# Kernel tuning notes

Hardware: AMD Instinct MI355X
Metric: run time of the kernel (lower is better)

The kernel has to match this reference:

```python
import jax, jax.numpy as jnp
import numpy as np

# dims
B, NB, T, NC = 16, 55, 512, 8          # batch, filter bands, time steps, CSP comps
D, L, H, E, K, F, C = 512, 6, 8, 8, 2, 2048, 2  # embed, depth, heads, experts, top_k, d_ff, classes
DH = D // H
IN = NB * NC  # 440
EPS = 1e-5


def _ln(x, s, b):
    m = x.mean(-1, keepdims=True)
    v = ((x - m) ** 2).mean(-1, keepdims=True)
    return (x - m) / jnp.sqrt(v + EPS) * s + b


def setup_inputs() -> dict:
    key = jax.random.key(0)
    ks = iter(jax.random.split(key, 64))
    n = lambda shape, s=0.02: jax.random.normal(next(ks), shape, jnp.float32) * s
    inp = {
        "x": jax.random.normal(next(ks), (B, NB, T, NC), jnp.float32),
        # frontend
        "proj_w": n((IN, D)), "proj_b": jnp.zeros((D,), jnp.float32),
        "pos": n((1, T, D)),
        "ln_pre_s": jnp.ones((D,), jnp.float32), "ln_pre_b": jnp.zeros((D,), jnp.float32),
        # stacked transformer-block params [L, ...]
        "ln1_s": jnp.ones((L, D), jnp.float32), "ln1_b": jnp.zeros((L, D), jnp.float32),
        "wq": n((L, D, D)), "bq": jnp.zeros((L, D), jnp.float32),
        "wk": n((L, D, D)), "bk": jnp.zeros((L, D), jnp.float32),
        "wv": n((L, D, D)), "bv": jnp.zeros((L, D), jnp.float32),
        "wo": n((L, D, D)), "bo": jnp.zeros((L, D), jnp.float32),
        "ln2_s": jnp.ones((L, D), jnp.float32), "ln2_b": jnp.zeros((L, D), jnp.float32),
        "gate_w": n((L, D, E)),
        "e_w1": n((L, E, D, F)), "e_b1": jnp.zeros((L, E, F), jnp.float32),
        "e_w2": n((L, E, F, D)), "e_b2": jnp.zeros((L, E, D), jnp.float32),
        # classifier head
        "ln_f_s": jnp.ones((D,), jnp.float32), "ln_f_b": jnp.zeros((D,), jnp.float32),
        "head_w": n((D, C)), "head_b": jnp.zeros((C,), jnp.float32),
    }
    return inp


def _moe(h, gw, w1, b1, w2, b2):
    # h: [N, D]; top-K softmax-gated mixture of GELU-FFN experts + load-balance aux loss
    N = h.shape[0]
    probs = jax.nn.softmax(h @ gw, axis=-1)                  # [N, E]
    vals, idx = jax.lax.top_k(probs, K)                      # [N, K]
    w = vals / vals.sum(-1, keepdims=True)                   # renormalized top-k weights
    disp = jax.nn.one_hot(idx, E, dtype=h.dtype)             # [N, K, E]
    combine = (disp * w[..., None]).sum(1)                   # [N, E]
    y = jnp.zeros_like(h)
    for e in range(E):  # small fixed expert loop
        y = y + combine[:, e:e + 1] * (jax.nn.gelu(h @ w1[e] + b1[e]) @ w2[e] + b2[e])
    frac = disp.mean((0, 1)) * K                             # fraction of tokens routed to each expert
    aux = E * jnp.sum(frac * probs.mean(0))
    return y, aux


def reference(x, proj_w, proj_b, pos, ln_pre_s, ln_pre_b, ln1_s, ln1_b, wq, bq, wk, bk,
              wv, bv, wo, bo, ln2_s, ln2_b, gate_w, e_w1, e_b1, e_w2, e_b2,
              ln_f_s, ln_f_b, head_w, head_b):
    b, nb, t, nc = x.shape
    h = x.transpose(0, 2, 1, 3).reshape(b, t, nb * nc) @ proj_w + proj_b  # [B,T,D]
    h = _ln(h + pos[:, :t, :], ln_pre_s, ln_pre_b)
    scale = DH ** -0.5
    total_aux = jnp.float32(0.0)
    for l in range(L):
        # pre-LN multi-head self-attention
        a = _ln(h, ln1_s[l], ln1_b[l])
        q = (a @ wq[l] + bq[l]).reshape(b, t, H, DH)
        k = (a @ wk[l] + bk[l]).reshape(b, t, H, DH)
        v = (a @ wv[l] + bv[l]).reshape(b, t, H, DH)
        att = jax.nn.softmax(jnp.einsum('bqhd,bkhd->bhqk', q, k) * scale, axis=-1)
        o = jnp.einsum('bhqk,bkhd->bqhd', att, v).reshape(b, t, D) @ wo[l] + bo[l]
        h = h + o
        # pre-LN MoE FFN
        m = _ln(h, ln2_s[l], ln2_b[l]).reshape(b * t, D)
        y, aux = _moe(m, gate_w[l], e_w1[l], e_b1[l], e_w2[l], e_b2[l])
        h = h + y.reshape(b, t, D)
        total_aux = total_aux + aux
    pooled = h.mean(axis=1)                                   # [B, D]
    logits = _ln(pooled, ln_f_s, ln_f_b) @ head_w + head_b    # [B, C]
    return logits, total_aux
```

## Files before the change

### kernel.cpp

```cpp
#include <hip/hip_runtime.h>
#include <stdint.h>

typedef unsigned short u16;
typedef unsigned int   u32;
typedef short bh8 __attribute__((ext_vector_type(8)));
typedef float f4  __attribute__((ext_vector_type(4)));

#define NTOK    8192
#define PADROWS 17408
#define MAXTILES 136

__device__ __forceinline__ u16 f2bf(float f){
  u32 u = __float_as_uint(f);
  return (u16)((u + 0x7fffu + ((u>>16)&1u)) >> 16);
}
__device__ __forceinline__ float bf2f(u16 h){ return __uint_as_float(((u32)h)<<16); }
__device__ __forceinline__ u32 pk2(float a, float b){ return (u32)f2bf(a) | ((u32)f2bf(b)<<16); }
__device__ __forceinline__ float gelu_f(float x){
  float u = 0.7978845608028654f*(x + 0.044715f*x*x*x);
  float t = 1.f - 2.f/(__expf(2.f*u)+1.f);
  return 0.5f*x*(1.f+t);
}
__device__ __forceinline__ void gload_lds16(const void* g, void* l){
  __builtin_amdgcn_global_load_lds((const __attribute__((address_space(1))) u32*)g,
                                   (__attribute__((address_space(3))) u32*)l, 16, 0, 0);
}

__global__ __launch_bounds__(256) void xpose_k(const float* __restrict__ x, u16* __restrict__ xt){
  int idx = blockIdx.x*256 + threadIdx.x;
  const float* src = x + (size_t)idx*8;
  float4 a = *(const float4*)src;
  float4 b = *(const float4*)(src+4);
  int t  = idx & 511;
  int nb = (idx>>9) % 55;
  int bb = (idx>>9) / 55;
  uint4 u;
  u.x = pk2(a.x,a.y); u.y = pk2(a.z,a.w); u.z = pk2(b.x,b.y); u.w = pk2(b.z,b.w);
  *(uint4*)&xt[((size_t)(bb*512+t))*448 + nb*8] = u;
}

__device__ __forceinline__ void tile_xpose(const float* __restrict__ src, u16* __restrict__ dst,
                                           int Ksrc, int N, int Kdst, float (*tile)[65])
{
  int tid = threadIdx.x;
  int k0 = blockIdx.y*64, n0 = blockIdx.x*64;
  #pragma unroll
  for (int p=0;p<4;++p){
    int r = p*16 + (tid>>4);
    int c4 = (tid&15)*4;
    int k = k0 + r;
    float4 v = (k < Ksrc) ? *(const float4*)&src[(size_t)k*N + n0 + c4] : (float4){0.f,0.f,0.f,0.f};
    tile[r][c4]=v.x; tile[r][c4+1]=v.y; tile[r][c4+2]=v.z; tile[r][c4+3]=v.w;
  }
  __syncthreads();
  #pragma unroll
  for (int p=0;p<2;++p){
    int rn = p*32 + (tid>>3);
    int ck = (tid&7)*8;
    uint4 u;
    u.x = pk2(tile[ck+0][rn], tile[ck+1][rn]);
    u.y = pk2(tile[ck+2][rn], tile[ck+3][rn]);
    u.z = pk2(tile[ck+4][rn], tile[ck+5][rn]);
    u.w = pk2(tile[ck+6][rn], tile[ck+7][rn]);
    *(uint4*)&dst[(size_t)(n0+rn)*Kdst + k0 + ck] = u;
  }
}

__global__ __launch_bounds__(256) void wconv_k(const float* __restrict__ src, u16* __restrict__ dst,
                                               int Ksrc, int N, int Kdst){
  __shared__ float tile[64][65];
  src += (size_t)blockIdx.z*Ksrc*N;
  dst += (size_t)blockIdx.z*N*Kdst;
  tile_xpose(src, dst, Ksrc, N, Kdst, tile);
}

__global__ __launch_bounds__(256) void wconv4_k(const float* __restrict__ wq, const float* __restrict__ wk,
    const float* __restrict__ wv, const float* __restrict__ wo,
    u16* __restrict__ qkvt, u16* __restrict__ wot)
{
  __shared__ float tile[64][65];
  int z = blockIdx.z;
  const float* src = (z==0)? wq : (z==1)? wk : (z==2)? wv : wo;
  u16* dst = (z==3) ? wot : qkvt + (size_t)z*512*512;
  tile_xpose(src, dst, 512, 512, 512, tile);
}

__global__ __launch_bounds__(256) void qkvb_k(const float* __restrict__ bq, const float* __restrict__ bk,
                                              const float* __restrict__ bv, float* __restrict__ qkvb){
  int idx = blockIdx.x*256 + threadIdx.x;
  int l = idx/1536, c = idx - l*1536;
  const float* s = (c<512)? bq : (c<1024)? bk : bv;
  qkvb[idx] = s[l*512 + (c&511)];
}

template<int MODE, bool GATHER>
__global__ __launch_bounds__(256) void gemm2_k(
    const u16* __restrict__ A, int lda,
    const u16* __restrict__ Bt, int ldb, int Ksteps,
    const float* __restrict__ biasBase,
    float* __restrict__ Cf, u16* __restrict__ Cb, int ldc,
    const int* __restrict__ tile_e, const int* __restrict__ toklist,
    const float* __restrict__ wlist, int expN)
{
  __shared__ __align__(16) u16 As[2][128*32];
  __shared__ __align__(16) u16 Bs[2][128*32];
  const int tid = threadIdx.x, lane = tid&63, w = tid>>6;
  const int wr = w>>1, wc = w&1;
  int nx = gridDim.x;
  int nwg = nx * gridDim.y;
  int lin = blockIdx.y*nx + blockIdx.x;
  int qq = nwg>>3, rr = nwg&7, xc = lin&7, oo = lin>>3;
  int wg = (xc<rr ? xc*(qq+1) : rr*(qq+1)+(xc-rr)*qq) + oo;
  int by = wg/nx, bx = wg - by*nx;
  const int n0 = bx*128, m0 = by*128;
  const u16* Bp = Bt;
  const float* bias = biasBase;
  if constexpr (MODE>=3){
    int e = tile_e[by];
    Bp   += (size_t)e*(size_t)expN*(size_t)ldb;
    bias += (size_t)e*(size_t)expN;
  }
  const u16* asrc0; const u16* asrc1; const u16* bsrc0; const u16* bsrc1;
  {
    int idx0 = tid, row0 = idx0>>2, sp0 = idx0&3, ks0 = sp0 ^ ((row0>>1)&3);
    int idx1 = 256+tid, row1 = idx1>>2, sp1 = idx1&3, ks1 = sp1 ^ ((row1>>1)&3);
    size_t ar0 = GATHER ? (size_t)toklist[m0+row0] : (size_t)(m0+row0);
    size_t ar1 = GATHER ? (size_t)toklist[m0+row1] : (size_t)(m0+row1);
    asrc0 = A + ar0*(size_t)lda + ks0*8;
    asrc1 = A + ar1*(size_t)lda + ks1*8;
    bsrc0 = Bp + (size_t)(n0+row0)*ldb + ks0*8;
    bsrc1 = Bp + (size_t)(n0+row1)*ldb + ks1*8;
  }
  f4 acc[4][4];
  #pragma unroll
  for (int i=0;i<4;++i)
    #pragma unroll
    for (int j=0;j<4;++j) acc[i][j] = (f4){0.f,0.f,0.f,0.f};

  gload_lds16(asrc0, &As[0][tid*8]);
  gload_lds16(asrc1, &As[0][(256+tid)*8]);
  gload_lds16(bsrc0, &Bs[0][tid*8]);
  gload_lds16(bsrc1, &Bs[0][(256+tid)*8]);
  asrc0 += 32; asrc1 += 32; bsrc0 += 32; bsrc1 += 32;
  __syncthreads();

  int buf = 0;
  for (int kt=0; kt<Ksteps; ++kt){
    if (kt+1 < Ksteps){
      int nb = buf^1;
      gload_lds16(asrc0, &As[nb][tid*8]);
      gload_lds16(asrc1, &As[nb][(256+tid)*8]);
      gload_lds16(bsrc0, &Bs[nb][tid*8]);
      gload_lds16(bsrc1, &Bs[nb][(256+tid)*8]);
      asrc0 += 32; asrc1 += 32; bsrc0 += 32; bsrc1 += 32;
    }
    bh8 af[4], bf[4];
    const int q = lane>>4;
    #pragma unroll
    for (int mf=0;mf<4;++mf){
      int r = wr*64 + mf*16 + (lane&15);
      af[mf] = *(const bh8*)&As[buf][r*32 + (q ^ ((r>>1)&3))*8];
    }
    #pragma unroll
    for (int nf=0;nf<4;++nf){
      int r = wc*64 + nf*16 + (lane&15);
      bf[nf] = *(const bh8*)&Bs[buf][r*32 + (q ^ ((r>>1)&3))*8];
    }
    #pragma unroll
    for (int mf=0;mf<4;++mf)
      #pragma unroll
      for (int nf=0;nf<4;++nf)
        acc[mf][nf] = __builtin_amdgcn_mfma_f32_16x16x32_bf16(af[mf], bf[nf], acc[mf][nf], 0, 0, 0);
    __syncthreads();
    buf ^= 1;
  }
  #pragma unroll
  for (int mf=0;mf<4;++mf){
    #pragma unroll
    for (int nf=0;nf<4;++nf){
      f4 d = acc[mf][nf];
      int ncol = n0 + wc*64 + nf*16 + (lane&15);
      float bv = bias[ncol];
      #pragma unroll
      for (int r=0;r<4;++r){
        int mrow = m0 + wr*64 + mf*16 + (lane>>4)*4 + r;
        float val = d[r] + bv;
        if constexpr (MODE==0){
          Cf[(size_t)mrow*ldc + ncol] = val;
        } else if constexpr (MODE==1){
          int slab = ncol>>6, dh = ncol&63;
          Cb[((size_t)slab*NTOK + (size_t)mrow)*64 + dh] = f2bf(val);
        } else if constexpr (MODE==2){
          Cf[(size_t)mrow*ldc + ncol] += val;
        } else if constexpr (MODE==3){
          Cb[(size_t)mrow*ldc + ncol] = f2bf(gelu_f(val));
        } else {
          Cb[(size_t)mrow*ldc + ncol] = f2bf(wlist[mrow]*val);
        }
      }
    }
  }
}

template<bool ADDPOS, bool OUTF32>
__global__ __launch_bounds__(256) void ln_k(const float* __restrict__ X, const float* __restrict__ pos,
    const float* __restrict__ sc, const float* __restrict__ bi,
    float* __restrict__ outF, u16* __restrict__ outB)
{
  int tid=threadIdx.x, lane=tid&63, w=tid>>6;
  int row = blockIdx.x*4 + w;
  const float* xr = X + (size_t)row*512 + lane*8;
  float x[8];
  float4 v0 = *(const float4*)xr;
  float4 v1 = *(const float4*)(xr+4);
  x[0]=v0.x;x[1]=v0.y;x[2]=v0.z;x[3]=v0.w;x[4]=v1.x;x[5]=v1.y;x[6]=v1.z;x[7]=v1.w;
  if constexpr (ADDPOS){
    const float* pr = pos + (size_t)(row&511)*512 + lane*8;
    float4 p0 = *(const float4*)pr, p1 = *(const float4*)(pr+4);
    x[0]+=p0.x;x[1]+=p0.y;x[2]+=p0.z;x[3]+=p0.w;x[4]+=p1.x;x[5]+=p1.y;x[6]+=p1.z;x[7]+=p1.w;
  }
  float sm=0.f, sq=0.f;
  #pragma unroll
  for (int i=0;i<8;++i){ sm+=x[i]; sq+=x[i]*x[i]; }
  #pragma unroll
  for (int mk=1; mk<64; mk<<=1){ sm += __shfl_xor(sm, mk); sq += __shfl_xor(sq, mk); }
  float mean = sm*(1.f/512.f);
  float var  = sq*(1.f/512.f) - mean*mean;
  float rstd = rsqrtf(var + 1e-5f);
  int d0 = lane*8;
  float4 s0 = *(const float4*)(sc+d0), s1 = *(const float4*)(sc+d0+4);
  float4 b0 = *(const float4*)(bi+d0), b1 = *(const float4*)(bi+d0+4);
  float y[8];
  y[0]=(x[0]-mean)*rstd*s0.x+b0.x; y[1]=(x[1]-mean)*rstd*s0.y+b0.y;
  y[2]=(x[2]-mean)*rstd*s0.z+b0.z; y[3]=(x[3]-mean)*rstd*s0.w+b0.w;
  y[4]=(x[4]-mean)*rstd*s1.x+b1.x; y[5]=(x[5]-mean)*rstd*s1.y+b1.y;
  y[6]=(x[6]-mean)*rstd*s1.z+b1.z; y[7]=(x[7]-mean)*rstd*s1.w+b1.w;
  if constexpr (OUTF32){
    float4 o0 = {y[0],y[1],y[2],y[3]}, o1 = {y[4],y[5],y[6],y[7]};
    *(float4*)(outF + (size_t)row*512 + d0)     = o0;
    *(float4*)(outF + (size_t)row*512 + d0 + 4) = o1;
  } else {
    uint4 u; u.x=pk2(y[0],y[1]); u.y=pk2(y[2],y[3]); u.z=pk2(y[4],y[5]); u.w=pk2(y[6],y[7]);
    *(uint4*)&outB[(size_t)row*512 + d0] = u;
  }
}

__global__ __launch_bounds__(256) void attn_k(const u16* __restrict__ QKV, u16* __restrict__ Og)
{
  __shared__ __align__(16) u16 VT[2][64*72];
  __shared__ __align__(16) u16 PS[4][16*72];
  int tid=threadIdx.x, lane=tid&63, w=tid>>6;
  int qt=blockIdx.x, hh=blockIdx.y, bb=blockIdx.z;
  const u16* Qh = QKV + ((size_t)hh     *NTOK + (size_t)bb*512)*64;
  const u16* Kh = QKV + ((size_t)(8+hh) *NTOK + (size_t)bb*512)*64;
  const u16* Vh = QKV + ((size_t)(16+hh)*NTOK + (size_t)bb*512)*64;
  size_t obase = (size_t)bb*512*512 + (size_t)hh*64;
  int qrow0 = qt*64 + w*16;
  bh8 qf[2];
  #pragma unroll
  for (int kf=0;kf<2;++kf)
    qf[kf] = *(const bh8*)&Qh[ (size_t)(qrow0 + (lane&15))*64 + kf*32 + (lane>>4)*8 ];
  f4 oacc[4];
  #pragma unroll
  for (int i=0;i<4;++i) oacc[i] = (f4){0.f,0.f,0.f,0.f};
  float mrun[4] = {-1e30f,-1e30f,-1e30f,-1e30f};
  float lrun[4] = {0.f,0.f,0.f,0.f};
  const float scale = 0.125f;

  for (int kt=0; kt<8; ++kt){
    const int buf = kt&1;
    #pragma unroll
    for (int r2=0;r2<2;++r2){
      int idx = r2*256 + tid;
      int dhg = idx&7;
      int dh0 = dhg*8, key = idx>>3;
      uint4 raw = *(const uint4*)&Vh[ (size_t)(kt*64+key)*64 + dh0 ];
      int kx = key ^ (dhg<<3);
      u32 rw[4] = {raw.x, raw.y, raw.z, raw.w};
      #pragma unroll
      for (int j=0;j<4;++j){
        VT[buf][(dh0+2*j  )*72 + kx] = (u16)(rw[j]&0xffff);
        VT[buf][(dh0+2*j+1)*72 + kx] = (u16)(rw[j]>>16);
      }
    }
    f4 s[4];
    #pragma unroll
    for (int nf=0;nf<4;++nf){
      size_t krow = (size_t)(kt*64+nf*16+(lane&15))*64 + (lane>>4)*8;
      bh8 k0 = *(const bh8*)&Kh[krow];
      bh8 k1 = *(const bh8*)&Kh[krow+32];
      f4 z = (f4){0.f,0.f,0.f,0.f};
      z = __builtin_amdgcn_mfma_f32_16x16x32_bf16(qf[0], k0, z, 0,0,0);
      z = __builtin_amdgcn_mfma_f32_16x16x32_bf16(qf[1], k1, z, 0,0,0);
      s[nf] = z;
    }
    float pe[4][4];
    #pragma unroll
    for (int r=0;r<4;++r){
      float sv0=s[0][r]*scale, sv1=s[1][r]*scale, sv2=s[2][r]*scale, sv3=s[3][r]*scale;
      float mt = fmaxf(fmaxf(sv0,sv1), fmaxf(sv2,sv3));
      #pragma unroll
      for (int mk=1; mk<16; mk<<=1) mt = fmaxf(mt, __shfl_xor(mt, mk));
      float mn = fmaxf(mrun[r], mt);
      float sf = __expf(mrun[r]-mn);
      float p0=__expf(sv0-mn), p1=__expf(sv1-mn), p2=__expf(sv2-mn), p3=__expf(sv3-mn);
      pe[0][r]=p0; pe[1][r]=p1; pe[2][r]=p2; pe[3][r]=p3;
      float rs = p0+p1+p2+p3;
      #pragma unroll
      for (int mk=1; mk<16; mk<<=1) rs += __shfl_xor(rs, mk);
      lrun[r] = lrun[r]*sf + rs;
      mrun[r] = mn;
      #pragma unroll
      for (int df=0;df<4;++df) oacc[df][r] *= sf;
    }
    #pragma unroll
    for (int nf=0;nf<4;++nf)
      #pragma unroll
      for (int r=0;r<4;++r)
        PS[w][ ((lane>>4)*4+r)*72 + nf*16 + (lane&15) ] = f2bf(pe[nf][r]);
    __syncthreads();
    #pragma unroll
    for (int ks=0;ks<2;++ks){
      bh8 pa = *(const bh8*)&PS[w][ (lane&15)*72 + ks*32 + (lane>>4)*8 ];
      #pragma unroll
      for (int df=0;df<4;++df){
        int dh = df*16 + (lane&15);
        int sgrp = (dh>>3)&7;
        bh8 vb = *(const bh8*)&VT[buf][ dh*72 + ((ks*4 + (lane>>4)) ^ sgrp)*8 ];
        oacc[df] = __builtin_amdgcn_mfma_f32_16x16x32_bf16(pa, vb, oacc[df], 0,0,0);
      }
    }
  }
  #pragma unroll
  for (int df=0;df<4;++df)
    #pragma unroll
    for (int r=0;r<4;++r){
      int qr = qrow0 + (lane>>4)*4 + r;
      float ov = oacc[df][r] / lrun[r];
      Og[ obase + (size_t)qr*512 + df*16 + (lane&15) ] = f2bf(ov);
    }
}

__global__ __launch_bounds__(256) void route_k(const u16* __restrict__ m, const float* __restrict__ gw,
    float* __restrict__ psum, int* __restrict__ cnt, int* __restrict__ t2e, float* __restrict__ t2w)
{
  __shared__ float ps[8]; __shared__ int cs[8];
  int tid=threadIdx.x, lane=tid&63, w=tid>>6;
  if (tid<8){ ps[tid]=0.f; cs[tid]=0; }
  __syncthreads();
  for (int it=0; it<4; ++it){
    int t = blockIdx.x*16 + w*4 + it;
    const u16* row = m + (size_t)t*512 + lane*8;
    uint4 raw = *(const uint4*)row;
    u32 rw[4] = {raw.x,raw.y,raw.z,raw.w};
    float x[8];
    #pragma unroll
    for (int j=0;j<4;++j){ x[2*j]=bf2f((u16)(rw[j]&0xffff)); x[2*j+1]=bf2f((u16)(rw[j]>>16)); }
    float acc[8] = {0,0,0,0,0,0,0,0};
    #pragma unroll
    for (int j=0;j<8;++j){
      const float* g = gw + (size_t)(lane*8+j)*8;
      float4 g0 = *(const float4*)g, g1 = *(const float4*)(g+4);
      acc[0]+=x[j]*g0.x; acc[1]+=x[j]*g0.y; acc[2]+=x[j]*g0.z; acc[3]+=x[j]*g0.w;
      acc[4]+=x[j]*g1.x; acc[5]+=x[j]*g1.y; acc[6]+=x[j]*g1.z; acc[7]+=x[j]*g1.w;
    }
    #pragma unroll
    for (int mk=1; mk<64; mk<<=1)
      #pragma unroll
      for (int e=0;e<8;++e) acc[e] += __shfl_xor(acc[e], mk);
    if (lane==0){
      float mx=acc[0];
      #pragma unroll
      for (int e=1;e<8;++e) mx = fmaxf(mx, acc[e]);
      float pe[8], tot=0.f;
      #pragma unroll
      for (int e=0;e<8;++e){ pe[e]=__expf(acc[e]-mx); tot+=pe[e]; }
      float inv = 1.f/tot;
      #pragma unroll
      for (int e=0;e<8;++e) pe[e]*=inv;
      int e0=0; float v0=pe[0];
      #pragma unroll
      for (int e=1;e<8;++e) if (pe[e]>v0){ v0=pe[e]; e0=e; }
      int e1=-1; float v1=-1.f;
      #pragma unroll
      for (int e=0;e<8;++e) if (e!=e0 && pe[e]>v1){ v1=pe[e]; e1=e; }
      float invw = 1.f/(v0+v1);
      t2e[2*t]=e0; t2w[2*t]=v0*invw; t2e[2*t+1]=e1; t2w[2*t+1]=v1*invw;
      #pragma unroll
      for (int e=0;e<8;++e) atomicAdd(&ps[e], pe[e]);
      atomicAdd(&cs[e0],1); atomicAdd(&cs[e1],1);
    }
  }
  __syncthreads();
  if (tid<8){ atomicAdd(&psum[tid], ps[tid]); atomicAdd(&cnt[tid], cs[tid]); }
}

__global__ __launch_bounds__(256) void offsets_k(const int* __restrict__ cnt, const float* __restrict__ psum,
    int* __restrict__ offs, int* __restrict__ fill, int* __restrict__ tile_e,
    int* __restrict__ toklist, float* __restrict__ wlist, float* __restrict__ auxp)
{
  int tid = threadIdx.x;
  if (tid==0){
    int off=0; float auxl=0.f;
    for (int e=0;e<8;++e){
      offs[e] = off;
      int reg = (cnt[e]+127)&~127;
      int t0 = off>>7, t1 = (off+reg)>>7;
      for (int t=t0;t<t1;++t) tile_e[t]=e;
      off += reg;
      auxl += ((float)cnt[e]*(1.f/8192.f)) * (psum[e]*(1.f/8192.f));
    }
    for (int t=off>>7; t<MAXTILES; ++t) tile_e[t]=0;
    auxp[0] += 8.f*auxl;
  }
  if (tid<8) fill[tid]=0;
  for (int i=tid;i<PADROWS;i+=256){ toklist[i]=0; wlist[i]=0.f; }
}

__global__ __launch_bounds__(256) void scatter_k(const int* __restrict__ t2e, const float* __restrict__ t2w,
    const int* __restrict__ offs, int* __restrict__ fill,
    int* __restrict__ toklist, float* __restrict__ wlist, int* __restrict__ t2pos)
{
  int t = blockIdx.x*256 + threadIdx.x;
  #pragma unroll
  for (int kk=0;kk<2;++kk){
    int e = t2e[2*t+kk];
    int p = atomicAdd(&fill[e], 1);
    int i = offs[e] + p;
    toklist[i] = t; wlist[i] = t2w[2*t+kk]; t2pos[2*t+kk] = i;
  }
}

__global__ __launch_bounds__(256) void gather_k(float* __restrict__ h, const u16* __restrict__ yb,
                                                const int* __restrict__ t2pos)
{
  int tid = threadIdx.x;
  int t = blockIdx.x*4 + (tid>>6);
  int lane = tid&63;
  int p0 = t2pos[2*t], p1 = t2pos[2*t+1];
  uint4 a = *(const uint4*)&yb[(size_t)p0*512 + lane*8];
  uint4 b = *(const uint4*)&yb[(size_t)p1*512 + lane*8];
  float* hp = h + (size_t)t*512 + lane*8;
  float4 h0 = *(float4*)hp, h1 = *(float4*)(hp+4);
  h0.x += bf2f((u16)(a.x&0xffff)) + bf2f((u16)(b.x&0xffff));
  h0.y += bf2f((u16)(a.x>>16))    + bf2f((u16)(b.x>>16));
  h0.z += bf2f((u16)(a.y&0xffff)) + bf2f((u16)(b.y&0xffff));
  h0.w += bf2f((u16)(a.y>>16))    + bf2f((u16)(b.y>>16));
  h1.x += bf2f((u16)(a.z&0xffff)) + bf2f((u16)(b.z&0xffff));
  h1.y += bf2f((u16)(a.z>>16))    + bf2f((u16)(b.z>>16));
  h1.z += bf2f((u16)(a.w&0xffff)) + bf2f((u16)(b.w&0xffff));
  h1.w += bf2f((u16)(a.w>>16))    + bf2f((u16)(b.w>>16));
  *(float4*)hp = h0; *(float4*)(hp+4) = h1;
}

__global__ __launch_bounds__(256) void pool_k(const float* __restrict__ h, float* __restrict__ pooled){
  int idx = blockIdx.x*256 + threadIdx.x;
  int bb = idx>>9, d = idx&511;
  const float* p = h + (size_t)bb*512*512 + d;
  float s=0.f;
  for (int t=0;t<512;++t) s += p[(size_t)t*512];
  pooled[idx] = s*(1.f/512.f);
}

__global__ __launch_bounds__(256) void head_k(const float* __restrict__ pooled,
    const float* __restrict__ sc, const float* __restrict__ bi,
    const float* __restrict__ hw, const float* __restrict__ hb,
    const float* __restrict__ auxp, float* __restrict__ out)
{
  int tid=threadIdx.x, lane=tid&63, w=tid>>6;
  for (int i=0;i<4;++i){
    int row = w*4+i;
    const float* xr = pooled + (size_t)row*512 + lane*8;
    float x[8];
    float4 v0 = *(const float4*)xr, v1 = *(const float4*)(xr+4);
    x[0]=v0.x;x[1]=v0.y;x[2]=v0.z;x[3]=v0.w;x[4]=v1.x;x[5]=v1.y;x[6]=v1.z;x[7]=v1.w;
    float sm=0.f, sq=0.f;
    #pragma unroll
    for (int j=0;j<8;++j){ sm+=x[j]; sq+=x[j]*x[j]; }
    #pragma unroll
    for (int mk=1; mk<64; mk<<=1){ sm += __shfl_xor(sm, mk); sq += __shfl_xor(sq, mk); }
    float mean = sm*(1.f/512.f);
    float rstd = rsqrtf(sq*(1.f/512.f) - mean*mean + 1e-5f);
    int d0 = lane*8;
    float c0=0.f, c1=0.f;
    #pragma unroll
    for (int j=0;j<8;++j){
      float yv = (x[j]-mean)*rstd*sc[d0+j] + bi[d0+j];
      c0 += yv*hw[(d0+j)*2]; c1 += yv*hw[(d0+j)*2+1];
    }
    #pragma unroll
    for (int mk=1; mk<64; mk<<=1){ c0 += __shfl_xor(c0, mk); c1 += __shfl_xor(c1, mk); }
    if (lane==0){ out[row*2+0] = c0 + hb[0]; out[row*2+1] = c1 + hb[1]; }
  }
  if (tid==0) out[32] = auxp[0];
}

extern "C" void kernel_launch(void* const* d_in, const int* in_sizes, int n_in,
                              void* d_out, int out_size, void* d_ws, size_t ws_size,
                              hipStream_t stream)
{
  (void)in_sizes; (void)n_in; (void)out_size; (void)ws_size;
  const float* x      = (const float*)d_in[0];
  const float* proj_w = (const float*)d_in[1];
  const float* proj_b = (const float*)d_in[2];
  const float* pos    = (const float*)d_in[3];
  const float* ln_pre_s=(const float*)d_in[4];
  const float* ln_pre_b=(const float*)d_in[5];
  const float* ln1_s  = (const float*)d_in[6];
  const float* ln1_b  = (const float*)d_in[7];
  const float* wq     = (const float*)d_in[8];
  const float* bq     = (const float*)d_in[9];
  const float* wk     = (const float*)d_in[10];
  const float* bk     = (const float*)d_in[11];
  const float* wv     = (const float*)d_in[12];
  const float* bv     = (const float*)d_in[13];
  const float* wo     = (const float*)d_in[14];
  const float* bo     = (const float*)d_in[15];
  const float* ln2_s  = (const float*)d_in[16];
  const float* ln2_b  = (const float*)d_in[17];
  const float* gate_w = (const float*)d_in[18];
  const float* e_w1   = (const float*)d_in[19];
  const float* e_b1   = (const float*)d_in[20];
  const float* e_w2   = (const float*)d_in[21];
  const float* e_b2   = (const float*)d_in[22];
  const float* ln_f_s = (const float*)d_in[23];
  const float* ln_f_b = (const float*)d_in[24];
  const float* head_w = (const float*)d_in[25];
  const float* head_b = (const float*)d_in[26];

  char* base = (char*)d_ws;
  size_t off = 0;
  auto carve = [&](size_t bytes)->char*{
    char* r = base + off; off += (bytes + 255) & ~(size_t)255; return r;
  };
  u16*   xt      = (u16*)  carve((size_t)8192*448*2);
  float* h       = (float*)carve((size_t)8192*512*4);
  u16*   a       = (u16*)  carve((size_t)8192*512*2);
  u16*   qkv     = (u16*)  carve((size_t)8192*1536*2);
  u16*   ob      = (u16*)  carve((size_t)8192*512*2);
  u16*   hidden  = (u16*)  carve((size_t)PADROWS*2048*2);
  u16*   ybuf    = (u16*)  carve((size_t)PADROWS*512*2);
  u16*   projt   = (u16*)  carve((size_t)512*448*2);
  u16*   qkvt    = (u16*)  carve((size_t)1536*512*2);
  u16*   wot     = (u16*)  carve((size_t)512*512*2);
  u16*   w1t     = (u16*)  carve((size_t)8*2048*512*2);
  u16*   w2t     = (u16*)  carve((size_t)8*512*2048*2);
  float* qkvb    = (float*)carve((size_t)6*1536*4);
  int*   toklist = (int*)  carve(PADROWS*4);
  float* wlist   = (float*)carve(PADROWS*4);
  int*   tile_e  = (int*)  carve(256*4);
  int*   rcntA   = (int*)  carve(6*16*4);
  int*   fill    = (int*)  carve(64);
  int*   offs    = (int*)  carve(64);
  int*   t2e     = (int*)  carve(16384*4);
  float* t2w     = (float*)carve(16384*4);
  int*   t2pos   = (int*)  carve(16384*4);
  float* pooled  = (float*)carve(8192*4);
  float* auxp    = (float*)carve(256);

  hipMemsetAsync(xt, 0, (size_t)8192*448*2, stream);
  hipMemsetAsync(rcntA, 0, 6*16*4, stream);
  hipMemsetAsync(auxp, 0, 4, stream);

  xpose_k<<<1760, 256, 0, stream>>>(x, xt);
  wconv_k<<<dim3(8,7,1), 256, 0, stream>>>(proj_w, projt, 440, 512, 448);
  qkvb_k<<<36, 256, 0, stream>>>(bq, bk, bv, qkvb);
  gemm2_k<0,false><<<dim3(4,64), 256, 0, stream>>>(xt, 448, projt, 448, 14, proj_b,
      h, nullptr, 512, nullptr, nullptr, nullptr, 0);
  ln_k<true,true><<<2048, 256, 0, stream>>>(h, pos, ln_pre_s, ln_pre_b, h, nullptr);

  for (int l=0; l<6; ++l){
    int*   cnt  = rcntA + l*16;
    float* psum = (float*)(cnt + 8);
    wconv4_k<<<dim3(8,8,4), 256, 0, stream>>>(wq+(size_t)l*512*512, wk+(size_t)l*512*512,
        wv+(size_t)l*512*512, wo+(size_t)l*512*512, qkvt, wot);
    ln_k<false,false><<<2048, 256, 0, stream>>>(h, nullptr, ln1_s+(size_t)l*512, ln1_b+(size_t)l*512, nullptr, a);
    gemm2_k<1,false><<<dim3(12,64), 256, 0, stream>>>(a, 512, qkvt, 512, 16, qkvb+(size_t)l*1536,
        nullptr, qkv, 1536, nullptr, nullptr, nullptr, 0);
    attn_k<<<dim3(8,8,16), 256, 0, stream>>>(qkv, ob);
    gemm2_k<2,false><<<dim3(4,64), 256, 0, stream>>>(ob, 512, wot, 512, 16, bo+(size_t)l*512,
        h, nullptr, 512, nullptr, nullptr, nullptr, 0);
    ln_k<false,false><<<2048, 256, 0, stream>>>(h, nullptr, ln2_s+(size_t)l*512, ln2_b+(size_t)l*512, nullptr, a);
    route_k<<<512, 256, 0, stream>>>(a, gate_w+(size_t)l*512*8, psum, cnt, t2e, t2w);
    offsets_k<<<1, 256, 0, stream>>>(cnt, psum, offs, fill, tile_e, toklist, wlist, auxp);
    scatter_k<<<32, 256, 0, stream>>>(t2e, t2w, offs, fill, toklist, wlist, t2pos);
    wconv_k<<<dim3(32,8,8), 256, 0, stream>>>(e_w1+(size_t)l*8*512*2048, w1t, 512, 2048, 512);
    wconv_k<<<dim3(8,32,8), 256, 0, stream>>>(e_w2+(size_t)l*8*2048*512, w2t, 2048, 512, 2048);
    gemm2_k<3,true ><<<dim3(16,MAXTILES), 256, 0, stream>>>(a, 512, w1t, 512, 16,
        e_b1 + (size_t)l*8*2048, nullptr, hidden, 2048, tile_e, toklist, wlist, 2048);
    gemm2_k<4,false><<<dim3(4,MAXTILES), 256, 0, stream>>>(hidden, 2048, w2t, 2048, 64,
        e_b2 + (size_t)l*8*512, nullptr, ybuf, 512, tile_e, nullptr, wlist, 512);
    gather_k<<<2048, 256, 0, stream>>>(h, ybuf, t2pos);
  }

  pool_k<<<32, 256, 0, stream>>>(h, pooled);
  head_k<<<1, 256, 0, stream>>>(pooled, ln_f_s, ln_f_b, head_w, head_b, auxp, (float*)d_out);
}
```

Measured before the change: 2.357 ms.

## Batch all weight conversions upfront and fuse gather/LN/routing kernels

Moves the per-layer weight transposes and bf16 conversions for all six layers into three batched launches before the layer loop, at the cost of larger weight buffers. Fuses the MoE gather with the next layer's LN1, and LN2 with the router, so activations are read fewer times and several launches disappear. The offsets kernel also clears the token lists with many blocks instead of one. This trades extra memory for fewer launches and less serial work on the per-layer critical path.

```diff
diff --git a/kernel.cpp b/kernel.cpp
--- a/kernel.cpp
+++ b/kernel.cpp
@@ -74,14 +74,16 @@
   tile_xpose(src, dst, Ksrc, N, Kdst, tile);
 }
 
-__global__ __launch_bounds__(256) void wconv4_k(const float* __restrict__ wq, const float* __restrict__ wk,
+__global__ __launch_bounds__(256) void wconvqkvo_k(const float* __restrict__ wq, const float* __restrict__ wk,
     const float* __restrict__ wv, const float* __restrict__ wo,
     u16* __restrict__ qkvt, u16* __restrict__ wot)
 {
   __shared__ float tile[64][65];
   int z = blockIdx.z;
-  const float* src = (z==0)? wq : (z==1)? wk : (z==2)? wv : wo;
-  u16* dst = (z==3) ? wot : qkvt + (size_t)z*512*512;
+  int l = z>>2, which = z&3;
+  const float* src = ((which==0)? wq : (which==1)? wk : (which==2)? wv : wo) + (size_t)l*512*512;
+  u16* dst = (which==3) ? wot + (size_t)l*512*512
+                        : qkvt + (size_t)l*1536*512 + (size_t)which*512*512;
   tile_xpose(src, dst, 512, 512, 512, tile);
 }
 
@@ -245,6 +247,47 @@
   }
 }
 
+__global__ __launch_bounds__(256) void gatherln_k(float* __restrict__ h,
+    const u16* __restrict__ yb, const int* __restrict__ t2pos,
+    const float* __restrict__ sc, const float* __restrict__ bi, u16* __restrict__ outB)
+{
+  int tid=threadIdx.x, lane=tid&63, w=tid>>6;
+  int row = blockIdx.x*4 + w;
+  float* hp = h + (size_t)row*512 + lane*8;
+  float4 v0 = *(float4*)hp, v1 = *(float4*)(hp+4);
+  int p0 = t2pos[2*row], p1 = t2pos[2*row+1];
+  uint4 ya = *(const uint4*)&yb[(size_t)p0*512 + lane*8];
+  uint4 yv = *(const uint4*)&yb[(size_t)p1*512 + lane*8];
+  float x[8];
+  x[0]=v0.x + bf2f((u16)(ya.x&0xffff)) + bf2f((u16)(yv.x&0xffff));
+  x[1]=v0.y + bf2f((u16)(ya.x>>16))    + bf2f((u16)(yv.x>>16));
+  x[2]=v0.z + bf2f((u16)(ya.y&0xffff)) + bf2f((u16)(yv.y&0xffff));
+  x[3]=v0.w + bf2f((u16)(ya.y>>16))    + bf2f((u16)(yv.y>>16));
+  x[4]=v1.x + bf2f((u16)(ya.z&0xffff)) + bf2f((u16)(yv.z&0xffff));
+  x[5]=v1.y + bf2f((u16)(ya.z>>16))    + bf2f((u16)(yv.z>>16));
+  x[6]=v1.z + bf2f((u16)(ya.w&0xffff)) + bf2f((u16)(yv.w&0xffff));
+  x[7]=v1.w + bf2f((u16)(ya.w>>16))    + bf2f((u16)(yv.w>>16));
+  float4 o0 = {x[0],x[1],x[2],x[3]}, o1 = {x[4],x[5],x[6],x[7]};
+  *(float4*)hp = o0; *(float4*)(hp+4) = o1;
+  float sm=0.f, sq=0.f;
+  #pragma unroll
+  for (int i=0;i<8;++i){ sm+=x[i]; sq+=x[i]*x[i]; }
+  #pragma unroll
+  for (int mk=1; mk<64; mk<<=1){ sm += __shfl_xor(sm, mk); sq += __shfl_xor(sq, mk); }
+  float mean = sm*(1.f/512.f);
+  float rstd = rsqrtf(sq*(1.f/512.f) - mean*mean + 1e-5f);
+  int d0 = lane*8;
+  float4 s0 = *(const float4*)(sc+d0), s1 = *(const float4*)(sc+d0+4);
+  float4 b0 = *(const float4*)(bi+d0), b1 = *(const float4*)(bi+d0+4);
+  float y[8];
+  y[0]=(x[0]-mean)*rstd*s0.x+b0.x; y[1]=(x[1]-mean)*rstd*s0.y+b0.y;
+  y[2]=(x[2]-mean)*rstd*s0.z+b0.z; y[3]=(x[3]-mean)*rstd*s0.w+b0.w;
+  y[4]=(x[4]-mean)*rstd*s1.x+b1.x; y[5]=(x[5]-mean)*rstd*s1.y+b1.y;
+  y[6]=(x[6]-mean)*rstd*s1.z+b1.z; y[7]=(x[7]-mean)*rstd*s1.w+b1.w;
+  uint4 u; u.x=pk2(y[0],y[1]); u.y=pk2(y[2],y[3]); u.z=pk2(y[4],y[5]); u.w=pk2(y[6],y[7]);
+  *(uint4*)&outB[(size_t)row*512 + d0] = u;
+}
+
 __global__ __launch_bounds__(256) void attn_k(const u16* __restrict__ QKV, u16* __restrict__ Og)
 {
   __shared__ __align__(16) u16 VT[2][64*72];
@@ -341,28 +384,45 @@
     }
 }
 
-__global__ __launch_bounds__(256) void route_k(const u16* __restrict__ m, const float* __restrict__ gw,
+__global__ __launch_bounds__(256) void lnroute_k(const float* __restrict__ h,
+    const float* __restrict__ sc, const float* __restrict__ bi, u16* __restrict__ outB,
+    const float* __restrict__ gw,
     float* __restrict__ psum, int* __restrict__ cnt, int* __restrict__ t2e, float* __restrict__ t2w)
 {
   __shared__ float ps[8]; __shared__ int cs[8];
   int tid=threadIdx.x, lane=tid&63, w=tid>>6;
   if (tid<8){ ps[tid]=0.f; cs[tid]=0; }
   __syncthreads();
+  int d0 = lane*8;
+  float4 s0 = *(const float4*)(sc+d0), s1 = *(const float4*)(sc+d0+4);
+  float4 b0 = *(const float4*)(bi+d0), b1 = *(const float4*)(bi+d0+4);
   for (int it=0; it<4; ++it){
     int t = blockIdx.x*16 + w*4 + it;
-    const u16* row = m + (size_t)t*512 + lane*8;
-    uint4 raw = *(const uint4*)row;
-    u32 rw[4] = {raw.x,raw.y,raw.z,raw.w};
+    const float* xr = h + (size_t)t*512 + d0;
     float x[8];
-    #pragma unroll
-    for (int j=0;j<4;++j){ x[2*j]=bf2f((u16)(rw[j]&0xffff)); x[2*j+1]=bf2f((u16)(rw[j]>>16)); }
+    float4 v0 = *(const float4*)xr, v1 = *(const float4*)(xr+4);
+    x[0]=v0.x;x[1]=v0.y;x[2]=v0.z;x[3]=v0.w;x[4]=v1.x;x[5]=v1.y;x[6]=v1.z;x[7]=v1.w;
+    float sm=0.f, sq=0.f;
+    #pragma unroll
+    for (int i=0;i<8;++i){ sm+=x[i]; sq+=x[i]*x[i]; }
+    #pragma unroll
+    for (int mk=1; mk<64; mk<<=1){ sm += __shfl_xor(sm, mk); sq += __shfl_xor(sq, mk); }
+    float mean = sm*(1.f/512.f);
+    float rstd = rsqrtf(sq*(1.f/512.f) - mean*mean + 1e-5f);
+    float y[8];
+    y[0]=(x[0]-mean)*rstd*s0.x+b0.x; y[1]=(x[1]-mean)*rstd*s0.y+b0.y;
+    y[2]=(x[2]-mean)*rstd*s0.z+b0.z; y[3]=(x[3]-mean)*rstd*s0.w+b0.w;
+    y[4]=(x[4]-mean)*rstd*s1.x+b1.x; y[5]=(x[5]-mean)*rstd*s1.y+b1.y;
+    y[6]=(x[6]-mean)*rstd*s1.z+b1.z; y[7]=(x[7]-mean)*rstd*s1.w+b1.w;
+    uint4 u; u.x=pk2(y[0],y[1]); u.y=pk2(y[2],y[3]); u.z=pk2(y[4],y[5]); u.w=pk2(y[6],y[7]);
+    *(uint4*)&outB[(size_t)t*512 + d0] = u;
     float acc[8] = {0,0,0,0,0,0,0,0};
     #pragma unroll
     for (int j=0;j<8;++j){
-      const float* g = gw + (size_t)(lane*8+j)*8;
+      const float* g = gw + (size_t)(d0+j)*8;
       float4 g0 = *(const float4*)g, g1 = *(const float4*)(g+4);
-      acc[0]+=x[j]*g0.x; acc[1]+=x[j]*g0.y; acc[2]+=x[j]*g0.z; acc[3]+=x[j]*g0.w;
-      acc[4]+=x[j]*g1.x; acc[5]+=x[j]*g1.y; acc[6]+=x[j]*g1.z; acc[7]+=x[j]*g1.w;
+      acc[0]+=y[j]*g0.x; acc[1]+=y[j]*g0.y; acc[2]+=y[j]*g0.z; acc[3]+=y[j]*g0.w;
+      acc[4]+=y[j]*g1.x; acc[5]+=y[j]*g1.y; acc[6]+=y[j]*g1.z; acc[7]+=y[j]*g1.w;
     }
     #pragma unroll
     for (int mk=1; mk<64; mk<<=1)
@@ -399,22 +459,25 @@
     int* __restrict__ offs, int* __restrict__ fill, int* __restrict__ tile_e,
     int* __restrict__ toklist, float* __restrict__ wlist, float* __restrict__ auxp)
 {
-  int tid = threadIdx.x;
-  if (tid==0){
-    int off=0; float auxl=0.f;
-    for (int e=0;e<8;++e){
-      offs[e] = off;
-      int reg = (cnt[e]+127)&~127;
-      int t0 = off>>7, t1 = (off+reg)>>7;
-      for (int t=t0;t<t1;++t) tile_e[t]=e;
-      off += reg;
-      auxl += ((float)cnt[e]*(1.f/8192.f)) * (psum[e]*(1.f/8192.f));
-    }
-    for (int t=off>>7; t<MAXTILES; ++t) tile_e[t]=0;
-    auxp[0] += 8.f*auxl;
-  }
-  if (tid<8) fill[tid]=0;
-  for (int i=tid;i<PADROWS;i+=256){ toklist[i]=0; wlist[i]=0.f; }
+  int tid = threadIdx.x, b = blockIdx.x;
+  int i = b*256 + tid;
+  if (i < PADROWS){ toklist[i]=0; wlist[i]=0.f; }
+  if (b==0){
+    if (tid==0){
+      int off=0; float auxl=0.f;
+      for (int e=0;e<8;++e){
+        offs[e] = off;
+        int reg = (cnt[e]+127)&~127;
+        int t0 = off>>7, t1 = (off+reg)>>7;
+        for (int t=t0;t<t1;++t) tile_e[t]=e;
+        off += reg;
+        auxl += ((float)cnt[e]*(1.f/8192.f)) * (psum[e]*(1.f/8192.f));
+      }
+      for (int t=off>>7; t<MAXTILES; ++t) tile_e[t]=0;
+      auxp[0] += 8.f*auxl;
+    }
+    if (tid<8) fill[tid]=0;
+  }
 }
 
 __global__ __launch_bounds__(256) void scatter_k(const int* __restrict__ t2e, const float* __restrict__ t2w,
@@ -541,10 +604,10 @@
   u16*   hidden  = (u16*)  carve((size_t)PADROWS*2048*2);
   u16*   ybuf    = (u16*)  carve((size_t)PADROWS*512*2);
   u16*   projt   = (u16*)  carve((size_t)512*448*2);
-  u16*   qkvt    = (u16*)  carve((size_t)1536*512*2);
-  u16*   wot     = (u16*)  carve((size_t)512*512*2);
-  u16*   w1t     = (u16*)  carve((size_t)8*2048*512*2);
-  u16*   w2t     = (u16*)  carve((size_t)8*512*2048*2);
+  u16*   qkvt    = (u16*)  carve((size_t)6*1536*512*2);
+  u16*   wot     = (u16*)  carve((size_t)6*512*512*2);
+  u16*   w1t     = (u16*)  carve((size_t)6*8*2048*512*2);
+  u16*   w2t     = (u16*)  carve((size_t)6*8*512*2048*2);
   float* qkvb    = (float*)carve((size_t)6*1536*4);
   int*   toklist = (int*)  carve(PADROWS*4);
   float* wlist   = (float*)carve(PADROWS*4);
@@ -564,6 +627,9 @@
 
   xpose_k<<<1760, 256, 0, stream>>>(x, xt);
   wconv_k<<<dim3(8,7,1), 256, 0, stream>>>(proj_w, projt, 440, 512, 448);
+  wconvqkvo_k<<<dim3(8,8,24), 256, 0, stream>>>(wq, wk, wv, wo, qkvt, wot);
+  wconv_k<<<dim3(32,8,48), 256, 0, stream>>>(e_w1, w1t, 512, 2048, 512);
+  wconv_k<<<dim3(8,32,48), 256, 0, stream>>>(e_w2, w2t, 2048, 512, 2048);
   qkvb_k<<<36, 256, 0, stream>>>(bq, bk, bv, qkvb);
   gemm2_k<0,false><<<dim3(4,64), 256, 0, stream>>>(xt, 448, projt, 448, 14, proj_b,
       h, nullptr, 512, nullptr, nullptr, nullptr, 0);
@@ -572,27 +638,27 @@
   for (int l=0; l<6; ++l){
     int*   cnt  = rcntA + l*16;
     float* psum = (float*)(cnt + 8);
-    wconv4_k<<<dim3(8,8,4), 256, 0, stream>>>(wq+(size_t)l*512*512, wk+(size_t)l*512*512,
-        wv+(size_t)l*512*512, wo+(size_t)l*512*512, qkvt, wot);
-    ln_k<false,false><<<2048, 256, 0, stream>>>(h, nullptr, ln1_s+(size_t)l*512, ln1_b+(size_t)l*512, nullptr, a);
-    gemm2_k<1,false><<<dim3(12,64), 256, 0, stream>>>(a, 512, qkvt, 512, 16, qkvb+(size_t)l*1536,
-        nullptr, qkv, 1536, nullptr, nullptr, nullptr, 0);
+    if (l == 0)
+      ln_k<false,false><<<2048, 256, 0, stream>>>(h, nullptr, ln1_s, ln1_b, nullptr, a);
+    else
+      gatherln_k<<<2048, 256, 0, stream>>>(h, ybuf, t2pos,
+          ln1_s+(size_t)l*512, ln1_b+(size_t)l*512, a);
+    gemm2_k<1,false><<<dim3(12,64), 256, 0, stream>>>(a, 512, qkvt+(size_t)l*1536*512, 512, 16,
+        qkvb+(size_t)l*1536, nullptr, qkv, 1536, nullptr, nullptr, nullptr, 0);
     attn_k<<<dim3(8,8,16), 256, 0, stream>>>(qkv, ob);
-    gemm2_k<2,false><<<dim3(4,64), 256, 0, stream>>>(ob, 512, wot, 512, 16, bo+(size_t)l*512,
-        h, nullptr, 512, nullptr, nullptr, nullptr, 0);
-    ln_k<false,false><<<2048, 256, 0, stream>>>(h, nullptr, ln2_s+(size_t)l*512, ln2_b+(size_t)l*512, nullptr, a);
-    route_k<<<512, 256, 0, stream>>>(a, gate_w+(size_t)l*512*8, psum, cnt, t2e, t2w);
-    offsets_k<<<1, 256, 0, stream>>>(cnt, psum, offs, fill, tile_e, toklist, wlist, auxp);
+    gemm2_k<2,false><<<dim3(4,64), 256, 0, stream>>>(ob, 512, wot+(size_t)l*512*512, 512, 16,
+        bo+(size_t)l*512, h, nullptr, 512, nullptr, nullptr, nullptr, 0);
+    lnroute_k<<<512, 256, 0, stream>>>(h, ln2_s+(size_t)l*512, ln2_b+(size_t)l*512, a,
+        gate_w+(size_t)l*512*8, psum, cnt, t2e, t2w);
+    offsets_k<<<68, 256, 0, stream>>>(cnt, psum, offs, fill, tile_e, toklist, wlist, auxp);
     scatter_k<<<32, 256, 0, stream>>>(t2e, t2w, offs, fill, toklist, wlist, t2pos);
-    wconv_k<<<dim3(32,8,8), 256, 0, stream>>>(e_w1+(size_t)l*8*512*2048, w1t, 512, 2048, 512);
-    wconv_k<<<dim3(8,32,8), 256, 0, stream>>>(e_w2+(size_t)l*8*2048*512, w2t, 2048, 512, 2048);
-    gemm2_k<3,true ><<<dim3(16,MAXTILES), 256, 0, stream>>>(a, 512, w1t, 512, 16,
+    gemm2_k<3,true ><<<dim3(16,MAXTILES), 256, 0, stream>>>(a, 512, w1t+(size_t)l*8*2048*512, 512, 16,
         e_b1 + (size_t)l*8*2048, nullptr, hidden, 2048, tile_e, toklist, wlist, 2048);
-    gemm2_k<4,false><<<dim3(4,MAXTILES), 256, 0, stream>>>(hidden, 2048, w2t, 2048, 64,
+    gemm2_k<4,false><<<dim3(4,MAXTILES), 256, 0, stream>>>(hidden, 2048, w2t+(size_t)l*8*512*2048, 2048, 64,
         e_b2 + (size_t)l*8*512, nullptr, ybuf, 512, tile_e, nullptr, wlist, 512);
-    gather_k<<<2048, 256, 0, stream>>>(h, ybuf, t2pos);
-  }
-
+  }
+
+  gather_k<<<2048, 256, 0, stream>>>(h, ybuf, t2pos);
   pool_k<<<32, 256, 0, stream>>>(h, pooled);
   head_k<<<1, 256, 0, stream>>>(pooled, ln_f_s, ln_f_b, head_w, head_b, auxp, (float*)d_out);
 }
```

Result: no change. 2.322 ms (-1.5%).
